# Optimization experiments

Measured on AMD Instinct MI355X. Metric: run time of the kernel, lower is better.

The kernel has to match this reference:

```python
import jax, jax.numpy as jnp
import numpy as np

N_NODES, N_EDGES = 50000, 800000
IN_DIM, OUT_DIM, EDGE_DIM = 128, 128, 32
NUM_HEADS = 8
HEAD_DIM = OUT_DIM // NUM_HEADS
SCALE = HEAD_DIM ** -0.5


def setup_inputs() -> dict:
    key = jax.random.key(0)
    ks = jax.random.split(key, 8)
    def lin_w(k, fan_in, fan_out):
        # kaiming-uniform-ish init like nn.Linear
        bound = 1.0 / np.sqrt(fan_in)
        return jax.random.uniform(k, (fan_in, fan_out), jnp.float32, -bound, bound)
    return {
        "node_features": jax.random.normal(ks[0], (N_NODES, IN_DIM), jnp.float32),
        "edge_features": jax.random.normal(ks[1], (N_EDGES, EDGE_DIM), jnp.float32),
        "Wq": lin_w(ks[2], IN_DIM, OUT_DIM), "bq": jnp.zeros((OUT_DIM,), jnp.float32),
        "Wk": lin_w(ks[3], IN_DIM, OUT_DIM), "bk": jnp.zeros((OUT_DIM,), jnp.float32),
        "Wv": lin_w(ks[4], IN_DIM, OUT_DIM), "bv": jnp.zeros((OUT_DIM,), jnp.float32),
        "We": lin_w(ks[5], EDGE_DIM, OUT_DIM), "be": jnp.zeros((OUT_DIM,), jnp.float32),
        "edge_list": jax.random.randint(ks[6], (N_EDGES, 2), 0, N_NODES, jnp.int32),
        "num_nodes": N_NODES,
    }


def reference(node_features, edge_features, Wq, bq, Wk, bk, Wv, bv, We, be, edge_list, num_nodes):
    # node projections -> [N, H, D]
    Q = (node_features @ Wq + bq).reshape(-1, NUM_HEADS, HEAD_DIM)
    K = (node_features @ Wk + bk).reshape(-1, NUM_HEADS, HEAD_DIM)
    V = (node_features @ Wv + bv).reshape(-1, NUM_HEADS, HEAD_DIM)
    edge_bias = (edge_features @ We + be).reshape(-1, NUM_HEADS, HEAD_DIM)

    src = edge_list[:, 0]  # node_in
    dst = edge_list[:, 1]  # node_out

    # per-edge per-head scores: [E, H]
    scores = jnp.einsum("ehd,ehd->eh", Q[src], K[dst]) * SCALE + edge_bias.sum(-1)
    # NOTE: softmax over the HEADS axis (dim=1), exactly as in the source
    weights = jax.nn.softmax(scores, axis=1)

    # weighted messages gathered from src, scattered to dst: [E, H, D] -> [N, H, D]
    msg = V[src] * weights[..., None]
    node_updates = jax.ops.segment_sum(msg, dst, num_segments=num_nodes)
    return node_updates.reshape(num_nodes, OUT_DIM)
```

## Files before the change

### kernel.cpp

```cpp
#include <hip/hip_runtime.h>
#include <math.h>

#define IN_DIM   128
#define OUT_DIM  128
#define EDGE_DIM 32
#define NUM_HEADS 8
#define HEAD_DIM 16
#define SCALE 0.25f
#define CSTRIDE 16
#define MAXDEG 48

typedef __attribute__((ext_vector_type(8))) short bf16x8;
typedef __attribute__((ext_vector_type(4))) float f32x4;
typedef __attribute__((ext_vector_type(2))) float f32x2;
typedef __attribute__((ext_vector_type(4))) unsigned int u32x4;

__device__ inline unsigned short f2bf(float x) {
    unsigned int u = __float_as_uint(x);
    unsigned int r = u + 0x7fff + ((u >> 16) & 1);
    return (unsigned short)(r >> 16);
}
__device__ inline float bflo(unsigned int u) { return __uint_as_float(u << 16); }
__device__ inline float bfhi(unsigned int u) { return __uint_as_float(u & 0xffff0000u); }
__device__ inline f32x2 up2(unsigned int u) {
    f32x2 r; r[0] = bflo(u); r[1] = bfhi(u); return r;
}

__global__ __launch_bounds__(256) void setup_kernel(
    int* __restrict__ counts, int n_nodes, int nbz,
    const float* __restrict__ Wq, const float* __restrict__ Wk,
    const float* __restrict__ Wv, unsigned short* __restrict__ WtB, int nbw,
    const float* __restrict__ We, const float* __restrict__ be,
    float* __restrict__ WeR, float* __restrict__ beR,
    const float* __restrict__ X, unsigned short* __restrict__ Xb)
{
    const int bx = blockIdx.x;
    const int t  = threadIdx.x;
    if (bx < nbz) {
        const int i = bx * 256 + t;
        if (i < n_nodes) counts[i << 4] = 0;
    } else if (bx < nbz + nbw) {
        const int idx = (bx - nbz) * 256 + t;
        const int mat = idx >> 14;
        const int rem = idx & 16383;
        const int n = rem >> 7, k = rem & 127;
        const float* W = (mat == 0) ? Wq : (mat == 1) ? Wk : Wv;
        WtB[mat * 16384 + n * 128 + k] = f2bf(W[k * 128 + n]);
    } else if (bx == nbz + nbw) {
        const int k = t >> 3, h = t & 7;
        float s = 0.f;
#pragma unroll
        for (int d = 0; d < HEAD_DIM; ++d) s += We[k * OUT_DIM + h * HEAD_DIM + d];
        WeR[k * NUM_HEADS + h] = s;
        if (t < NUM_HEADS) {
            float sb = 0.f;
#pragma unroll
            for (int d = 0; d < HEAD_DIM; ++d) sb += be[t * HEAD_DIM + d];
            beR[t] = sb;
        }
    } else {
        const int i = (bx - (nbz + nbw + 1)) * 256 + t;
        if (i < n_nodes * 16) {
            const f32x4* xr = (const f32x4*)(X + (size_t)i * 8);
            const f32x4 x0 = xr[0], x1 = xr[1];
            u32x4 p;
            p[0] = (unsigned)f2bf(x0[0]) | ((unsigned)f2bf(x0[1]) << 16);
            p[1] = (unsigned)f2bf(x0[2]) | ((unsigned)f2bf(x0[3]) << 16);
            p[2] = (unsigned)f2bf(x1[0]) | ((unsigned)f2bf(x1[1]) << 16);
            p[3] = (unsigned)f2bf(x1[2]) | ((unsigned)f2bf(x1[3]) << 16);
            *(u32x4*)(Xb + (size_t)i * 8) = p;
        }
    }
}

__global__ __launch_bounds__(256) void mega_kernel(
    const unsigned short* __restrict__ Xb, const unsigned short* __restrict__ WtB,
    const float* __restrict__ bq, const float* __restrict__ bk,
    const float* __restrict__ bv,
    unsigned short* __restrict__ QVb, unsigned short* __restrict__ Kb,
    int n_nodes, int nbq,
    const int* __restrict__ el, int* __restrict__ counts,
    const float* __restrict__ ef, const float* __restrict__ WeR,
    const float* __restrict__ beR, unsigned int* __restrict__ recs,
    int n_edges)
{
    __shared__ unsigned short stg[4][16][136];
    const int bx = blockIdx.x;
    const int t  = threadIdx.x;

    if (bx >= nbq) {
        const int e = (bx - nbq) * 256 + t;
        if (e >= n_edges) return;
        const int2 ed = ((const int2*)el)[e];
        const int r = atomicAdd(&counts[ed.y << 4], 1);

        float acc[NUM_HEADS];
#pragma unroll
        for (int h = 0; h < NUM_HEADS; ++h) acc[h] = beR[h];

        const f32x4* efr = (const f32x4*)(ef + (size_t)e * EDGE_DIM);
#pragma unroll
        for (int kk = 0; kk < 8; ++kk) {
            const f32x4 f = efr[kk];
#pragma unroll
            for (int c = 0; c < 4; ++c) {
                const float* wr = WeR + (kk * 4 + c) * NUM_HEADS;
#pragma unroll
                for (int h = 0; h < NUM_HEADS; ++h)
                    acc[h] = fmaf(f[c], wr[h], acc[h]);
            }
        }

        if (r < MAXDEG) {
            u32x4 r0, r1;
            r0[0] = (unsigned)ed.x;
            r0[1] = 0;
            r0[2] = (unsigned)f2bf(acc[0]) | ((unsigned)f2bf(acc[1]) << 16);
            r0[3] = (unsigned)f2bf(acc[2]) | ((unsigned)f2bf(acc[3]) << 16);
            r1[0] = (unsigned)f2bf(acc[4]) | ((unsigned)f2bf(acc[5]) << 16);
            r1[1] = (unsigned)f2bf(acc[6]) | ((unsigned)f2bf(acc[7]) << 16);
            r1[2] = 0; r1[3] = 0;
            u32x4* rp = (u32x4*)(recs + (size_t)(ed.y * MAXDEG + r) * 8);
            rp[0] = r0;
            rp[1] = r1;
        }
        return;
    }

    const int wave = t >> 6, lane = t & 63;
    const int quad = lane >> 4, li = lane & 15;
    const int m0 = bx * 64 + wave * 16;
    int mrow = m0 + li;
    if (mrow >= n_nodes) mrow = n_nodes - 1;

    bf16x8 a[4];
#pragma unroll
    for (int ks = 0; ks < 4; ++ks)
        a[ks] = *(const bf16x8*)(Xb + (size_t)mrow * 128 + ks * 32 + quad * 8);

    const int R = lane >> 2;
    const int cc4 = lane & 3;
    const int node = m0 + R;

#pragma unroll
    for (int which = 0; which < 3; ++which) {
        const float* bias = (which == 0) ? bq : (which == 1) ? bk : bv;
        const unsigned short* Wg = WtB + which * 16384;

        f32x4 acc[8];
#pragma unroll
        for (int nt = 0; nt < 8; ++nt) acc[nt] = (f32x4){0.f, 0.f, 0.f, 0.f};

#pragma unroll
        for (int ks = 0; ks < 4; ++ks) {
#pragma unroll
            for (int nt = 0; nt < 8; ++nt) {
                const bf16x8 b = *(const bf16x8*)(Wg + (nt * 16 + li) * 128 + ks * 32 + quad * 8);
                acc[nt] = __builtin_amdgcn_mfma_f32_16x16x32_bf16(a[ks], b, acc[nt], 0, 0, 0);
            }
        }

#pragma unroll
        for (int nt = 0; nt < 8; ++nt) {
            const float bb = bias[nt * 16 + li];
#pragma unroll
            for (int r = 0; r < 4; ++r)
                stg[wave][quad * 4 + r][nt * 16 + li] = f2bf(acc[nt][r] + bb);
        }
        __syncthreads();

        if (node < n_nodes) {
            const u32x4* s = (const u32x4*)(&stg[wave][R][cc4 * 32]);
            u32x4 d0 = s[0], d1 = s[1], d2 = s[2], d3 = s[3];
            unsigned short* dp =
                (which == 0) ? (QVb + (size_t)node * 256 + cc4 * 32)
              : (which == 1) ? (Kb  + (size_t)node * 128 + cc4 * 32)
              :                (QVb + (size_t)node * 256 + 128 + cc4 * 32);
            u32x4* d = (u32x4*)dp;
            d[0] = d0; d[1] = d1; d[2] = d2; d[3] = d3;
        }
        __syncthreads();
    }
}

__global__ __launch_bounds__(256) void aggregate_kernel(
    const unsigned short* __restrict__ QVb, const unsigned short* __restrict__ Kb,
    const int* __restrict__ counts, const unsigned int* __restrict__ recs,
    float* __restrict__ out, int n_nodes, int nwtot)
{
    const int lane = threadIdx.x & 63;
    const int g = lane >> 3;
    const int h = lane & 7;
    const int ebd = 2 + (h >> 1);

    int node = (blockIdx.x * 256 + threadIdx.x) >> 6;
    if (node >= n_nodes) return;
    int cnt = counts[node << 4];
    if (cnt > MAXDEG) cnt = MAXDEG;

    for (;;) {
        const int nnode = node + nwtot;
        int ncnt = 0;
        if (nnode < n_nodes) {
            ncnt = counts[nnode << 4];
            if (ncnt > MAXDEG) ncnt = MAXDEG;
        }

        const int beg = node * MAXDEG;

        f32x2 kf[8];
        {
            const u32x4* kp = (const u32x4*)(Kb + (size_t)node * 128 + h * 16);
            const u32x4 ka = kp[0], kb_ = kp[1];
#pragma unroll
            for (int j = 0; j < 4; ++j) { kf[j] = up2(ka[j]); kf[4 + j] = up2(kb_[j]); }
        }

        f32x2 acc[8];
#pragma unroll
        for (int j = 0; j < 8; ++j) acc[j] = (f32x2){0.f, 0.f};

        if (cnt > 0) {
            const int last = cnt - 1;
            int s0 = g; if (s0 > last) s0 = last;
            const unsigned src_c = recs[(size_t)(beg + s0) * 8];
            unsigned ebw_c = recs[(size_t)(beg + s0) * 8 + ebd];
            const unsigned short* bp0 = QVb + (size_t)src_c * 256 + h * 16;
            u32x4 qa = *(const u32x4*)bp0;
            u32x4 qb = *(const u32x4*)(bp0 + 8);
            u32x4 va = *(const u32x4*)(bp0 + 128);
            u32x4 vb = *(const u32x4*)(bp0 + 136);
            int s1 = 8 + g; if (s1 > last) s1 = last;
            unsigned src_n = recs[(size_t)(beg + s1) * 8];
            unsigned ebw_n = recs[(size_t)(beg + s1) * 8 + ebd];

            for (int i = 0; i < cnt; i += 8) {
                int s2 = i + 16 + g; if (s2 > last) s2 = last;
                const unsigned src_f = recs[(size_t)(beg + s2) * 8];
                const unsigned ebw_f = recs[(size_t)(beg + s2) * 8 + ebd];
                const unsigned short* bp = QVb + (size_t)src_n * 256 + h * 16;
                const u32x4 qan = *(const u32x4*)bp;
                const u32x4 qbn = *(const u32x4*)(bp + 8);
                const u32x4 van = *(const u32x4*)(bp + 128);
                const u32x4 vbn = *(const u32x4*)(bp + 136);

                const float eb = (h & 1) ? bfhi(ebw_c) : bflo(ebw_c);
                f32x2 p2 = (f32x2){0.f, 0.f};
#pragma unroll
                for (int j = 0; j < 4; ++j) {
                    p2 += up2(qa[j]) * kf[j];
                    p2 += up2(qb[j]) * kf[4 + j];
                }
                const float score = fmaf(p2[0] + p2[1], SCALE, eb);

                const float ex = __expf(score);
                float den = ex;
                den += __shfl_xor(den, 1);
                den += __shfl_xor(den, 2);
                den += __shfl_xor(den, 4);
                float wgt = __fdividef(ex, den);
                if (i + g >= cnt) wgt = 0.f;
                const f32x2 w2 = (f32x2){wgt, wgt};
#pragma unroll
                for (int j = 0; j < 4; ++j) {
                    acc[j]     += up2(va[j]) * w2;
                    acc[4 + j] += up2(vb[j]) * w2;
                }

                qa = qan; qb = qbn; va = van; vb = vbn;
                ebw_c = ebw_n;
                src_n = src_f; ebw_n = ebw_f;
            }
        }

#pragma unroll
        for (int mask = 8; mask <= 32; mask <<= 1)
#pragma unroll
            for (int j = 0; j < 8; ++j) {
                f32x2 o;
                o[0] = __shfl_xor(acc[j][0], mask);
                o[1] = __shfl_xor(acc[j][1], mask);
                acc[j] += o;
            }

        float ox = 0.f, oy = 0.f;
#pragma unroll
        for (int j = 0; j < 8; ++j)
            if (g == j) { ox = acc[j][0]; oy = acc[j][1]; }
        *(float2*)(out + (size_t)node * OUT_DIM + h * 16 + g * 2) = make_float2(ox, oy);

        if (nnode >= n_nodes) break;
        node = nnode; cnt = ncnt;
    }
}

extern "C" void kernel_launch(void* const* d_in, const int* in_sizes, int n_in,
                              void* d_out, int out_size, void* d_ws, size_t ws_size,
                              hipStream_t stream)
{
    const float* X   = (const float*)d_in[0];
    const float* ef  = (const float*)d_in[1];
    const float* Wq  = (const float*)d_in[2];
    const float* bq  = (const float*)d_in[3];
    const float* Wk  = (const float*)d_in[4];
    const float* bk  = (const float*)d_in[5];
    const float* Wv  = (const float*)d_in[6];
    const float* bv  = (const float*)d_in[7];
    const float* We  = (const float*)d_in[8];
    const float* be  = (const float*)d_in[9];
    const int*   el  = (const int*)d_in[10];

    const int n_nodes = in_sizes[0] / IN_DIM;
    const int n_edges = in_sizes[10] / 2;

    char* w = (char*)d_ws;
    auto alloc = [&](size_t bytes) { char* p = w; w += (bytes + 255) & ~(size_t)255; return p; };

    unsigned short* QVb  = (unsigned short*)alloc((size_t)n_nodes * 256 * 2);
    unsigned short* Kb   = (unsigned short*)alloc((size_t)n_nodes * 128 * 2);
    unsigned short* WtB  = (unsigned short*)alloc((size_t)3 * 128 * 128 * 2);
    unsigned int*   recs = (unsigned int*)alloc((size_t)n_nodes * MAXDEG * 32);
    unsigned short* Xb   = (unsigned short*)alloc((size_t)n_nodes * 128 * 2);
    float* WeR   = (float*)alloc(EDGE_DIM * NUM_HEADS * 4);
    float* beR   = (float*)alloc(NUM_HEADS * 4);
    int* counts  = (int*)alloc((size_t)n_nodes * CSTRIDE * 4);

    const int nbz = (n_nodes + 255) / 256;
    const int nbw = (3 * 128 * 128) / 256;
    const int nbx = (n_nodes * 16 + 255) / 256;
    setup_kernel<<<nbz + nbw + 1 + nbx, 256, 0, stream>>>(
        counts, n_nodes, nbz, Wq, Wk, Wv, WtB, nbw, We, be, WeR, beR, X, Xb);

    const int nbq = (n_nodes + 63) / 64;
    const int nbh = (n_edges + 255) / 256;
    mega_kernel<<<nbq + nbh, 256, 0, stream>>>(
        Xb, WtB, bq, bk, bv, QVb, Kb, n_nodes, nbq,
        el, counts, ef, WeR, beR, recs, n_edges);

    int nblk = (n_nodes + 3) / 4;
    if (nblk > 2048) nblk = 2048;
    aggregate_kernel<<<nblk, 256, 0, stream>>>(
        QVb, Kb, counts, recs, (float*)d_out, n_nodes, nblk * 4);
}
```

Before: 332.6 us.

## Fuse node-feature bf16 conversion into projection GEMM and reorder mega-kernel blocks

Drops the separate pass in setup_kernel that converted node features to a bf16 buffer. The GEMM part of mega_kernel now loads fp32 X directly and converts it to bf16 in registers, which removes one write and one read of the intermediate array. The block order in mega_kernel is also flipped so the edge-processing blocks, which do atomics and scattered writes, are scheduled before the GEMM blocks. The cost is twice as many bytes read per X element inside the GEMM, plus conversion ALU work on the GEMM path.

After: 341.5 us. 1.03x slower.

```diff
diff --git a/kernel.cpp b/kernel.cpp
--- a/kernel.cpp
+++ b/kernel.cpp
@@ -31,8 +31,7 @@
     const float* __restrict__ Wq, const float* __restrict__ Wk,
     const float* __restrict__ Wv, unsigned short* __restrict__ WtB, int nbw,
     const float* __restrict__ We, const float* __restrict__ be,
-    float* __restrict__ WeR, float* __restrict__ beR,
-    const float* __restrict__ X, unsigned short* __restrict__ Xb)
+    float* __restrict__ WeR, float* __restrict__ beR)
 {
     const int bx = blockIdx.x;
     const int t  = threadIdx.x;
@@ -46,7 +45,7 @@
         const int n = rem >> 7, k = rem & 127;
         const float* W = (mat == 0) ? Wq : (mat == 1) ? Wk : Wv;
         WtB[mat * 16384 + n * 128 + k] = f2bf(W[k * 128 + n]);
-    } else if (bx == nbz + nbw) {
+    } else {
         const int k = t >> 3, h = t & 7;
         float s = 0.f;
 #pragma unroll
@@ -58,27 +57,15 @@
             for (int d = 0; d < HEAD_DIM; ++d) sb += be[t * HEAD_DIM + d];
             beR[t] = sb;
         }
-    } else {
-        const int i = (bx - (nbz + nbw + 1)) * 256 + t;
-        if (i < n_nodes * 16) {
-            const f32x4* xr = (const f32x4*)(X + (size_t)i * 8);
-            const f32x4 x0 = xr[0], x1 = xr[1];
-            u32x4 p;
-            p[0] = (unsigned)f2bf(x0[0]) | ((unsigned)f2bf(x0[1]) << 16);
-            p[1] = (unsigned)f2bf(x0[2]) | ((unsigned)f2bf(x0[3]) << 16);
-            p[2] = (unsigned)f2bf(x1[0]) | ((unsigned)f2bf(x1[1]) << 16);
-            p[3] = (unsigned)f2bf(x1[2]) | ((unsigned)f2bf(x1[3]) << 16);
-            *(u32x4*)(Xb + (size_t)i * 8) = p;
-        }
     }
 }
 
 __global__ __launch_bounds__(256) void mega_kernel(
-    const unsigned short* __restrict__ Xb, const unsigned short* __restrict__ WtB,
+    const float* __restrict__ X, const unsigned short* __restrict__ WtB,
     const float* __restrict__ bq, const float* __restrict__ bk,
     const float* __restrict__ bv,
     unsigned short* __restrict__ QVb, unsigned short* __restrict__ Kb,
-    int n_nodes, int nbq,
+    int n_nodes, int nbh,
     const int* __restrict__ el, int* __restrict__ counts,
     const float* __restrict__ ef, const float* __restrict__ WeR,
     const float* __restrict__ beR, unsigned int* __restrict__ recs,
@@ -88,8 +75,8 @@
     const int bx = blockIdx.x;
     const int t  = threadIdx.x;
 
-    if (bx >= nbq) {
-        const int e = (bx - nbq) * 256 + t;
+    if (bx < nbh) {
+        const int e = bx * 256 + t;
         if (e >= n_edges) return;
         const int2 ed = ((const int2*)el)[e];
         const int r = atomicAdd(&counts[ed.y << 4], 1);
@@ -127,16 +114,25 @@
         return;
     }
 
+    const int gb = bx - nbh;
     const int wave = t >> 6, lane = t & 63;
     const int quad = lane >> 4, li = lane & 15;
-    const int m0 = bx * 64 + wave * 16;
+    const int m0 = gb * 64 + wave * 16;
     int mrow = m0 + li;
     if (mrow >= n_nodes) mrow = n_nodes - 1;
 
     bf16x8 a[4];
 #pragma unroll
-    for (int ks = 0; ks < 4; ++ks)
-        a[ks] = *(const bf16x8*)(Xb + (size_t)mrow * 128 + ks * 32 + quad * 8);
+    for (int ks = 0; ks < 4; ++ks) {
+        const f32x4* xr = (const f32x4*)(X + (size_t)mrow * 128 + ks * 32 + quad * 8);
+        const f32x4 x0 = xr[0], x1 = xr[1];
+        bf16x8 av;
+        av[0] = (short)f2bf(x0[0]); av[1] = (short)f2bf(x0[1]);
+        av[2] = (short)f2bf(x0[2]); av[3] = (short)f2bf(x0[3]);
+        av[4] = (short)f2bf(x1[0]); av[5] = (short)f2bf(x1[1]);
+        av[6] = (short)f2bf(x1[2]); av[7] = (short)f2bf(x1[3]);
+        a[ks] = av;
+    }
 
     const int R = lane >> 2;
     const int cc4 = lane & 3;
@@ -320,21 +316,19 @@
     unsigned short* Kb   = (unsigned short*)alloc((size_t)n_nodes * 128 * 2);
     unsigned short* WtB  = (unsigned short*)alloc((size_t)3 * 128 * 128 * 2);
     unsigned int*   recs = (unsigned int*)alloc((size_t)n_nodes * MAXDEG * 32);
-    unsigned short* Xb   = (unsigned short*)alloc((size_t)n_nodes * 128 * 2);
     float* WeR   = (float*)alloc(EDGE_DIM * NUM_HEADS * 4);
     float* beR   = (float*)alloc(NUM_HEADS * 4);
     int* counts  = (int*)alloc((size_t)n_nodes * CSTRIDE * 4);
 
     const int nbz = (n_nodes + 255) / 256;
     const int nbw = (3 * 128 * 128) / 256;
-    const int nbx = (n_nodes * 16 + 255) / 256;
-    setup_kernel<<<nbz + nbw + 1 + nbx, 256, 0, stream>>>(
-        counts, n_nodes, nbz, Wq, Wk, Wv, WtB, nbw, We, be, WeR, beR, X, Xb);
-
+    setup_kernel<<<nbz + nbw + 1, 256, 0, stream>>>(
+        counts, n_nodes, nbz, Wq, Wk, Wv, WtB, nbw, We, be, WeR, beR);
+
+    const int nbh = (n_edges + 255) / 256;
     const int nbq = (n_nodes + 63) / 64;
-    const int nbh = (n_edges + 255) / 256;
-    mega_kernel<<<nbq + nbh, 256, 0, stream>>>(
-        Xb, WtB, bq, bk, bv, QVb, Kb, n_nodes, nbq,
+    mega_kernel<<<nbh + nbq, 256, 0, stream>>>(
+        X, WtB, bq, bk, bv, QVb, Kb, n_nodes, nbh,
         el, counts, ef, WeR, beR, recs, n_edges);
 
     int nblk = (n_nodes + 3) / 4;
```
